# Optimization experiments

Measured on AMD Instinct MI355X. Metric: run time of the kernel, lower is better.

## Reference

```python
import jax, jax.numpy as jnp
import numpy as np


def setup_inputs() -> dict:
    key = jax.random.key(0)
    k1, k2 = jax.random.split(key)
    N, T, D = 65536, 128, 2
    source = jax.random.normal(k1, (N, T, D), dtype=jnp.float32)
    mask = jax.random.randint(k2, (N, T, D), 0, 2).astype(jnp.float32)
    # Fixed (non-trainable) inertia-model matrices, as in the torch module.
    A = jnp.array([[0.0, 0.0, -1.0, 0.0],
                   [0.0, 0.0, 0.0, -1.0],
                   [0.0, 0.0, 0.0, 0.0],
                   [0.0, 0.0, 0.0, 0.0]], dtype=jnp.float32)
    B = jnp.array([[1.0, 0.0, 1.0, 0.0],
                   [0.0, 1.0, 0.0, 1.0]], dtype=jnp.float32)
    C = jnp.array([[0.0, 0.0],
                   [0.0, 0.0],
                   [1.0, 0.0],
                   [0.0, 1.0]], dtype=jnp.float32)
    return {"source": source, "mask": mask, "A": A, "B": B, "C": C,
            "burn_in_steps": 64}


def reference(source, mask, A, B, C, burn_in_steps):
    # use_mask=True variant of the Inertia model.
    N, T, D = source.shape
    state_dim = 4
    burn_in = int(burn_in_steps)

    src_t = jnp.swapaxes(source, 0, 1)  # [T, N, D]
    msk_t = jnp.swapaxes(mask, 0, 1)    # [T, N, D]
    ts = jnp.arange(T)

    s0 = jnp.zeros((N, state_dim), dtype=source.dtype)
    m0 = jnp.zeros((N, D), dtype=source.dtype)
    y0 = jnp.zeros((N, D), dtype=source.dtype)  # never used on first step

    def step(carry, inp):
        s, m, y = carry
        x_t, mask_t, t = inp
        in_burn = (burn_in <= 0) | (t < burn_in)  # scalar bool
        m_prev = m
        m_new = jnp.where(in_burn, mask_t, m)     # mask only advances in burn-in
        s_app = (1.0 - m_prev) * m_new            # [N, 2]
        x = jnp.where(in_burn, x_t, y)
        s_temp = s @ A + x @ B                    # [N, 4]
        s_next = jnp.concatenate(
            [s_temp[:, :2],
             s[:, 2:4] * s_app + s_temp[:, 2:4] * (1.0 - s_app)], axis=1)
        del_x = s_next @ C                        # [N, 2]
        y_new = x + del_x
        return (s_next, m_new, y_new), y_new

    _, pred = jax.lax.scan(step, (s0, m0, y0), (src_t, msk_t, ts))
    return jnp.swapaxes(pred, 0, 1)  # [N, T, D]
```

## Files before the change

### kernel.cpp

```cpp
#include <hip/hip_runtime.h>


__global__ __launch_bounds__(256) void inertia_scan(
    const float* __restrict__ src, const float* __restrict__ msk,
    float* __restrict__ out, int nseq)
{
    const int n = (blockIdx.x * 256 + threadIdx.x) >> 6;
    const int lane = threadIdx.x & 63;
    if (n >= nseq) return;
    const size_t base = (size_t)n * 128;
    const float2* __restrict__ s2 = (const float2*)src + base;
    const float2* __restrict__ m2 = (const float2*)msk + base;
    float2* __restrict__ o2 = (float2*)out + base;

    float2 sv = s2[lane];
    float2 mv = m2[lane];

    float spx = __shfl_up(sv.x, 1, 64);
    float spy = __shfl_up(sv.y, 1, 64);
    float mpx = __shfl_up(mv.x, 1, 64);
    float mpy = __shfl_up(mv.y, 1, 64);
    const bool l0 = (lane == 0);
    spx = l0 ? 0.f : spx;  spy = l0 ? 0.f : spy;
    mpx = l0 ? 0.f : mpx;  mpy = l0 ? 0.f : mpy;

    float A0 = (1.f - mpx) * mv.x;
    float A1 = (1.f - mpy) * mv.y;
    float B0 = (sv.x - spx) * (1.f - A0);
    float B1 = (sv.y - spy) * (1.f - A1);

#pragma unroll
    for (int off = 1; off < 64; off <<= 1) {
        float Ap0 = __shfl_up(A0, off, 64);
        float Bp0 = __shfl_up(B0, off, 64);
        float Ap1 = __shfl_up(A1, off, 64);
        float Bp1 = __shfl_up(B1, off, 64);
        const bool act = (lane >= off);
        Ap0 = act ? Ap0 : 1.f;  Bp0 = act ? Bp0 : 0.f;
        Ap1 = act ? Ap1 : 1.f;  Bp1 = act ? Bp1 : 0.f;
        B0 = fmaf(Bp0, A0, B0);  A0 *= Ap0;
        B1 = fmaf(Bp1, A1, B1);  A1 *= Ap1;
    }

    const float y0 = sv.x + B0;
    const float y1 = sv.y + B1;
    o2[lane] = make_float2(y0, y1);

    const float q63x = __shfl(B0, 63, 64);
    const float q63y = __shfl(B1, 63, 64);
    const float y63x = __shfl(y0, 63, 64);
    const float y63y = __shfl(y1, 63, 64);
    const float tj = (float)(lane + 1);
    o2[64 + lane] = make_float2(fmaf(tj, q63x, y63x), fmaf(tj, q63y, y63y));
}

extern "C" void kernel_launch(void* const* d_in, const int* in_sizes, int n_in,
                              void* d_out, int out_size, void* d_ws, size_t ws_size,
                              hipStream_t stream) {
    const float* src = (const float*)d_in[0];
    const float* msk = (const float*)d_in[1];
    float* out = (float*)d_out;
    const int nseq = in_sizes[0] / 256;
    const int block = 256;
    const int grid = (nseq + 3) / 4;
    inertia_scan<<<grid, block, 0, stream>>>(src, msk, out, nseq);
}
```

Before: 160.3 us.

## Process two sequences per wave with two timesteps per lane via float4

Each 64-lane wave now handles two sequences, one per 32-lane half, and each lane covers two consecutive timesteps loaded as float4. The pair of timesteps is composed locally into one affine step before the shuffle scan, so the scan needs five levels instead of six and a half-wave width. A small fix-up pass then recovers the per-timestep outputs. This halves the wave count and uses wider memory accesses, at the cost of more per-lane arithmetic on a kernel that is probably memory-bound.

```diff
diff --git a/kernel.cpp b/kernel.cpp
--- a/kernel.cpp
+++ b/kernel.cpp
@@ -1,57 +1,78 @@
 #include <hip/hip_runtime.h>
 
 
-__global__ __launch_bounds__(256) void inertia_scan(
+__global__ __launch_bounds__(256) void inertia_scan2(
     const float* __restrict__ src, const float* __restrict__ msk,
     float* __restrict__ out, int nseq)
 {
-    const int n = (blockIdx.x * 256 + threadIdx.x) >> 6;
+    const int wave = (blockIdx.x * 256 + threadIdx.x) >> 6;
     const int lane = threadIdx.x & 63;
+    const int half = lane >> 5;
+    const int l    = lane & 31;
+    const int n = 2 * wave + half;
     if (n >= nseq) return;
-    const size_t base = (size_t)n * 128;
-    const float2* __restrict__ s2 = (const float2*)src + base;
-    const float2* __restrict__ m2 = (const float2*)msk + base;
-    float2* __restrict__ o2 = (float2*)out + base;
+    const size_t idx = (size_t)n * 64 + l;
+    const float4* __restrict__ s4 = (const float4*)src;
+    const float4* __restrict__ m4 = (const float4*)msk;
+    float4* __restrict__ o4 = (float4*)out;
 
-    float2 sv = s2[lane];
-    float2 mv = m2[lane];
+    const float4 sv = s4[idx];
+    const float4 mv = m4[idx];
 
-    float spx = __shfl_up(sv.x, 1, 64);
-    float spy = __shfl_up(sv.y, 1, 64);
-    float mpx = __shfl_up(mv.x, 1, 64);
-    float mpy = __shfl_up(mv.y, 1, 64);
-    const bool l0 = (lane == 0);
-    spx = l0 ? 0.f : spx;  spy = l0 ? 0.f : spy;
-    mpx = l0 ? 0.f : mpx;  mpy = l0 ? 0.f : mpy;
+    float spz = __shfl_up(sv.z, 1, 32);
+    float spw = __shfl_up(sv.w, 1, 32);
+    float mpz = __shfl_up(mv.z, 1, 32);
+    float mpw = __shfl_up(mv.w, 1, 32);
+    const bool l0 = (l == 0);
+    spz = l0 ? 0.f : spz;  spw = l0 ? 0.f : spw;
+    mpz = l0 ? 0.f : mpz;  mpw = l0 ? 0.f : mpw;
 
-    float A0 = (1.f - mpx) * mv.x;
-    float A1 = (1.f - mpy) * mv.y;
-    float B0 = (sv.x - spx) * (1.f - A0);
-    float B1 = (sv.y - spy) * (1.f - A1);
+    const float aE0 = (1.f - mpz) * mv.x;
+    const float aE1 = (1.f - mpw) * mv.y;
+    const float bE0 = (sv.x - spz) * (1.f - aE0);
+    const float bE1 = (sv.y - spw) * (1.f - aE1);
+    const float aO0 = (1.f - mv.x) * mv.z;
+    const float aO1 = (1.f - mv.y) * mv.w;
+    const float bO0 = (sv.z - sv.x) * (1.f - aO0);
+    const float bO1 = (sv.w - sv.y) * (1.f - aO1);
+
+    float A0 = aO0 * aE0, B0 = fmaf(bE0, aO0, bO0);
+    float A1 = aO1 * aE1, B1 = fmaf(bE1, aO1, bO1);
 
 #pragma unroll
-    for (int off = 1; off < 64; off <<= 1) {
-        float Ap0 = __shfl_up(A0, off, 64);
-        float Bp0 = __shfl_up(B0, off, 64);
-        float Ap1 = __shfl_up(A1, off, 64);
-        float Bp1 = __shfl_up(B1, off, 64);
-        const bool act = (lane >= off);
+    for (int off = 1; off < 32; off <<= 1) {
+        float Ap0 = __shfl_up(A0, off, 32);
+        float Bp0 = __shfl_up(B0, off, 32);
+        float Ap1 = __shfl_up(A1, off, 32);
+        float Bp1 = __shfl_up(B1, off, 32);
+        const bool act = (l >= off);
         Ap0 = act ? Ap0 : 1.f;  Bp0 = act ? Bp0 : 0.f;
         Ap1 = act ? Ap1 : 1.f;  Bp1 = act ? Bp1 : 0.f;
         B0 = fmaf(Bp0, A0, B0);  A0 *= Ap0;
         B1 = fmaf(Bp1, A1, B1);  A1 *= Ap1;
     }
 
-    const float y0 = sv.x + B0;
-    const float y1 = sv.y + B1;
-    o2[lane] = make_float2(y0, y1);
+    float qp0 = __shfl_up(B0, 1, 32);
+    float qp1 = __shfl_up(B1, 1, 32);
+    qp0 = l0 ? 0.f : qp0;
+    qp1 = l0 ? 0.f : qp1;
 
-    const float q63x = __shfl(B0, 63, 64);
-    const float q63y = __shfl(B1, 63, 64);
-    const float y63x = __shfl(y0, 63, 64);
-    const float y63y = __shfl(y1, 63, 64);
-    const float tj = (float)(lane + 1);
-    o2[64 + lane] = make_float2(fmaf(tj, q63x, y63x), fmaf(tj, q63y, y63y));
+    const float qe0 = fmaf(aE0, qp0, bE0);
+    const float qe1 = fmaf(aE1, qp1, bE1);
+    const float qo0 = fmaf(aO0, qe0, bO0);
+    const float qo1 = fmaf(aO1, qe1, bO1);
+    o4[idx] = make_float4(sv.x + qe0, sv.y + qe1, sv.z + qo0, sv.w + qo1);
+
+    const float q63x = __shfl(B0, 31, 32);
+    const float q63y = __shfl(B1, 31, 32);
+    const float x63x = __shfl(sv.z, 31, 32);
+    const float x63y = __shfl(sv.w, 31, 32);
+    const float y63x = x63x + q63x;
+    const float y63y = x63y + q63y;
+    const float j0 = (float)(2 * l + 1);
+    const float j1 = (float)(2 * l + 2);
+    o4[idx + 32] = make_float4(fmaf(j0, q63x, y63x), fmaf(j0, q63y, y63y),
+                               fmaf(j1, q63x, y63x), fmaf(j1, q63y, y63y));
 }
 
 extern "C" void kernel_launch(void* const* d_in, const int* in_sizes, int n_in,
@@ -62,6 +83,6 @@
     float* out = (float*)d_out;
     const int nseq = in_sizes[0] / 256;
     const int block = 256;
-    const int grid = (nseq + 3) / 4;
-    inertia_scan<<<grid, block, 0, stream>>>(src, msk, out, nseq);
+    const int grid = (nseq + 7) / 8;
+    inertia_scan2<<<grid, block, 0, stream>>>(src, msk, out, nseq);
 }
```

Result: no change. 163.1 us (+1.7%).
